# Kernel tuning notes

Hardware: AMD Instinct MI355X
Metric: run time of the kernel (lower is better)

Reference implementation:

```python
import jax, jax.numpy as jnp
import numpy as np

N_NODES = 50000
N_EDGES = 800000
D = 256


def setup_inputs() -> dict:
    key = jax.random.key(0)
    k1, k2, k3 = jax.random.split(key, 3)
    node_features = jax.random.normal(k1, (N_NODES, D), dtype=jnp.float32)
    edge_index = jax.random.randint(k2, (2, N_EDGES), 0, N_NODES, dtype=jnp.int64)
    # GCNConv linear weight (glorot-ish scale) and bias
    W = jax.random.normal(k3, (D, D), dtype=jnp.float32) * (1.0 / np.sqrt(D))
    b = jnp.zeros((D,), dtype=jnp.float32)
    alpha = jnp.full((1,), 0.5, dtype=jnp.float32)
    return {"node_features": node_features, "edge_index": edge_index, "W": W, "b": b, "alpha": alpha}


def _gcn_conv(x, edge_index, W, b):
    # PyG GCNConv: add self-loops, symmetric deg^{-1/2} normalization,
    # x' = W x, out[i] = sum_{j in N(i)} norm_ij * x'_j + b
    N = x.shape[0]
    loop = jnp.arange(N, dtype=edge_index.dtype)
    src = jnp.concatenate([edge_index[0], loop])  # [E+N]
    dst = jnp.concatenate([edge_index[1], loop])
    deg = jax.ops.segment_sum(jnp.ones(src.shape, dtype=x.dtype), dst, num_segments=N)
    dinv = jnp.where(deg > 0, jax.lax.rsqrt(jnp.maximum(deg, 1.0)), 0.0)
    norm = dinv[src] * dinv[dst]  # [E+N]
    h = x @ W.T  # [N, D]
    msg = h[src] * norm[:, None]  # gather + scale
    out = jax.ops.segment_sum(msg, dst, num_segments=N)  # scatter-add to targets
    return out + b


def reference(node_features, edge_index, W, b, alpha):
    updated = _gcn_conv(node_features, edge_index, W, b)
    a = alpha[0]
    # eval mode: dropout = identity; alpha-weighted residual blend
    return a * node_features + (1.0 - a) * updated
```

## Files before the change

### kernel.cpp

```cpp
#include <hip/hip_runtime.h>

#define N_NODES 50000
#define N_EDGES 800000
#define D 256
#define SLOT 64
#define GEMM_BLOCKS 391
#define FILL_BLOCKS 1563

typedef unsigned short bf16_t;
typedef __attribute__((ext_vector_type(8))) short short8;
typedef __attribute__((ext_vector_type(8))) unsigned short ushort8_t;
typedef __attribute__((ext_vector_type(4))) float f32x4;

__device__ inline float b2f(bf16_t u) {
    union { float f; unsigned v; } t; t.v = ((unsigned)u) << 16; return t.f;
}
__device__ inline bf16_t f2b(float f) {
    union { float f; unsigned v; } t; t.f = f;
    unsigned u = t.v;
    return (bf16_t)((u + 0x7FFFu + ((u >> 16) & 1u)) >> 16);
}
__device__ inline unsigned cvt_pk_bf16(float lo, float hi) {
    unsigned r;
    asm("v_cvt_pk_bf16_f32 %0, %1, %2" : "=v"(r) : "v"(lo), "v"(hi));
    return r;
}
__device__ inline short8 cvt8(float4 a, float4 b) {
    union { short8 s; unsigned u[4]; } t;
    t.u[0] = cvt_pk_bf16(a.x, a.y);
    t.u[1] = cvt_pk_bf16(a.z, a.w);
    t.u[2] = cvt_pk_bf16(b.x, b.y);
    t.u[3] = cvt_pk_bf16(b.z, b.w);
    return t.s;
}

__global__ void initcur_kernel(int* __restrict__ cursor) {
    int i = blockIdx.x * 256 + threadIdx.x;
    if (i < N_NODES) cursor[i] = i << 6;
}

__global__ __launch_bounds__(512) void k1_kernel(const float* __restrict__ x,
                                                 const float* __restrict__ W,
                                                 bf16_t* __restrict__ h,
                                                 const int* __restrict__ ei,
                                                 int* __restrict__ cursor,
                                                 int* __restrict__ csr_src) {
    __shared__ __align__(16) bf16_t As[128 * 32];
    __shared__ __align__(16) bf16_t Bs[256 * 32];

    const int tid = threadIdx.x;

    if (blockIdx.x >= GEMM_BLOCKS) {
        int e = (blockIdx.x - GEMM_BLOCKS) * 512 + tid;
        if (e < N_EDGES) {
            int s = ei[e];
            int d = ei[N_EDGES + e];
            if ((unsigned)d < (unsigned)N_NODES) {
                int pos = atomicAdd(&cursor[d], 1);
                csr_src[pos] = s;
            }
        }
        return;
    }

    const int wid  = tid >> 6;
    const int lane = tid & 63;
    const int wr = wid >> 2;
    const int wc = wid & 3;
    const int row0 = blockIdx.x * 128;
    const int lr = lane & 15;
    const int lk = (lane >> 4) * 8;

    const int srow = tid >> 2;
    const int sq   = tid & 3;
    int sr = row0 + srow;
    if (sr >= N_NODES) sr = N_NODES - 1;
    const float* agp = &x[(size_t)sr * D + sq * 8];
    bf16_t* alp = &As[srow * 32 + sq * 8];

    float4 areg[16];
#pragma unroll
    for (int s = 0; s < 8; s++) {
        const float4* p = reinterpret_cast<const float4*>(&agp[s * 32]);
        areg[2 * s]     = p[0];
        areg[2 * s + 1] = p[1];
    }

    f32x4 acc[4][4] = {};

#pragma unroll
    for (int s = 0; s < 8; s++) {
        *reinterpret_cast<short8*>(alp) = cvt8(areg[2 * s], areg[2 * s + 1]);
#pragma unroll
        for (int j = 0; j < 2; j++) {
            int brow = (j * 512 + tid) >> 2;
            const float4* q = reinterpret_cast<const float4*>(&W[(size_t)brow * D + s * 32 + sq * 8]);
            float4 w0 = q[0], w1 = q[1];
            *reinterpret_cast<short8*>(&Bs[brow * 32 + sq * 8]) = cvt8(w0, w1);
        }
        __syncthreads();

        short8 a[4], b[4];
#pragma unroll
        for (int m = 0; m < 4; m++)
            a[m] = *reinterpret_cast<const short8*>(&As[(wr * 64 + m * 16 + lr) * 32 + lk]);
#pragma unroll
        for (int n = 0; n < 4; n++)
            b[n] = *reinterpret_cast<const short8*>(&Bs[(wc * 64 + n * 16 + lr) * 32 + lk]);
#pragma unroll
        for (int m = 0; m < 4; m++)
#pragma unroll
            for (int n = 0; n < 4; n++)
                acc[m][n] = __builtin_amdgcn_mfma_f32_16x16x32_bf16(a[m], b[n], acc[m][n], 0, 0, 0);
        __syncthreads();
    }

#pragma unroll
    for (int m = 0; m < 4; m++) {
        int rbase = row0 + wr * 64 + m * 16 + (lane >> 4) * 4;
#pragma unroll
        for (int j = 0; j < 4; j++) {
            int rr = rbase + j;
            if (rr < N_NODES) {
#pragma unroll
                for (int n = 0; n < 4; n++)
                    h[(size_t)rr * D + wc * 64 + n * 16 + lr] = f2b(acc[m][n][j]);
            }
        }
    }
}

__global__ void dinv_kernel(const int* __restrict__ cursor, float* __restrict__ dinv) {
    int i = blockIdx.x * 256 + threadIdx.x;
    if (i < N_NODES) {
        int cnt = cursor[i] - (i << 6);
        dinv[i] = rsqrtf((float)(cnt + 1));
    }
}

__global__ __launch_bounds__(256) void gather_kernel(const int* __restrict__ cursor,
                                                     const int* __restrict__ csr_src,
                                                     const float* __restrict__ dinv,
                                                     const bf16_t* __restrict__ h,
                                                     const float* __restrict__ x,
                                                     const float* __restrict__ b,
                                                     const float* __restrict__ alpha,
                                                     float* __restrict__ out) {
    const int half = (threadIdx.x >> 5) & 1;
    const int wv   = threadIdx.x >> 6;
    const int ln   = threadIdx.x & 31;
    const int n = blockIdx.x * 8 + wv * 2 + half;
    if (n >= N_NODES) return;
    const int col = ln * 8;

    const int beg = n << 6;
    const int end = cursor[n];
    const float dn = dinv[n];
    const bf16_t* hl = h + col;

    float a0 = 0.f, a1 = 0.f, a2 = 0.f, a3 = 0.f,
          a4 = 0.f, a5 = 0.f, a6 = 0.f, a7 = 0.f;
    int k = beg;
    for (; k + 3 < end; k += 4) {
        int s0 = csr_src[k], s1 = csr_src[k + 1], s2 = csr_src[k + 2], s3 = csr_src[k + 3];
        float n0 = dinv[s0] * dn, n1 = dinv[s1] * dn, n2 = dinv[s2] * dn, n3 = dinv[s3] * dn;
        ushort8_t r0 = *reinterpret_cast<const ushort8_t*>(&hl[(size_t)s0 * D]);
        ushort8_t r1 = *reinterpret_cast<const ushort8_t*>(&hl[(size_t)s1 * D]);
        ushort8_t r2 = *reinterpret_cast<const ushort8_t*>(&hl[(size_t)s2 * D]);
        ushort8_t r3 = *reinterpret_cast<const ushort8_t*>(&hl[(size_t)s3 * D]);
        a0 += b2f(r0[0]) * n0 + b2f(r1[0]) * n1 + b2f(r2[0]) * n2 + b2f(r3[0]) * n3;
        a1 += b2f(r0[1]) * n0 + b2f(r1[1]) * n1 + b2f(r2[1]) * n2 + b2f(r3[1]) * n3;
        a2 += b2f(r0[2]) * n0 + b2f(r1[2]) * n1 + b2f(r2[2]) * n2 + b2f(r3[2]) * n3;
        a3 += b2f(r0[3]) * n0 + b2f(r1[3]) * n1 + b2f(r2[3]) * n2 + b2f(r3[3]) * n3;
        a4 += b2f(r0[4]) * n0 + b2f(r1[4]) * n1 + b2f(r2[4]) * n2 + b2f(r3[4]) * n3;
        a5 += b2f(r0[5]) * n0 + b2f(r1[5]) * n1 + b2f(r2[5]) * n2 + b2f(r3[5]) * n3;
        a6 += b2f(r0[6]) * n0 + b2f(r1[6]) * n1 + b2f(r2[6]) * n2 + b2f(r3[6]) * n3;
        a7 += b2f(r0[7]) * n0 + b2f(r1[7]) * n1 + b2f(r2[7]) * n2 + b2f(r3[7]) * n3;
    }
    for (; k < end; k++) {
        int s0 = csr_src[k];
        float n0 = dinv[s0] * dn;
        ushort8_t r0 = *reinterpret_cast<const ushort8_t*>(&hl[(size_t)s0 * D]);
        a0 += b2f(r0[0]) * n0; a1 += b2f(r0[1]) * n0;
        a2 += b2f(r0[2]) * n0; a3 += b2f(r0[3]) * n0;
        a4 += b2f(r0[4]) * n0; a5 += b2f(r0[5]) * n0;
        a6 += b2f(r0[6]) * n0; a7 += b2f(r0[7]) * n0;
    }

    const float dv2 = dn * dn;
    const float a   = alpha[0];
    ushort8_t hv = *reinterpret_cast<const ushort8_t*>(&hl[(size_t)n * D]);
    const float4* xp = reinterpret_cast<const float4*>(&x[(size_t)n * D + col]);
    const float4* bp = reinterpret_cast<const float4*>(&b[col]);
    float4 xv0 = xp[0], xv1 = xp[1];
    float4 bv0 = bp[0], bv1 = bp[1];
    float4 r0, r1;
    r0.x = a * xv0.x + (1.0f - a) * (a0 + dv2 * b2f(hv[0]) + bv0.x);
    r0.y = a * xv0.y + (1.0f - a) * (a1 + dv2 * b2f(hv[1]) + bv0.y);
    r0.z = a * xv0.z + (1.0f - a) * (a2 + dv2 * b2f(hv[2]) + bv0.z);
    r0.w = a * xv0.w + (1.0f - a) * (a3 + dv2 * b2f(hv[3]) + bv0.w);
    r1.x = a * xv1.x + (1.0f - a) * (a4 + dv2 * b2f(hv[4]) + bv1.x);
    r1.y = a * xv1.y + (1.0f - a) * (a5 + dv2 * b2f(hv[5]) + bv1.y);
    r1.z = a * xv1.z + (1.0f - a) * (a6 + dv2 * b2f(hv[6]) + bv1.z);
    r1.w = a * xv1.w + (1.0f - a) * (a7 + dv2 * b2f(hv[7]) + bv1.w);
    float4* op = reinterpret_cast<float4*>(&out[(size_t)n * D + col]);
    op[0] = r0;
    op[1] = r1;
}

extern "C" void kernel_launch(void* const* d_in, const int* in_sizes, int n_in,
                              void* d_out, int out_size, void* d_ws, size_t ws_size,
                              hipStream_t stream) {
    const float* x     = (const float*)d_in[0];
    const int*   ei    = (const int*)d_in[1];
    const float* W     = (const float*)d_in[2];
    const float* b     = (const float*)d_in[3];
    const float* alpha = (const float*)d_in[4];
    float* out = (float*)d_out;

    char* ws = (char*)d_ws;
    const size_t HB = (size_t)N_NODES * D * 2;
    bf16_t* h      = (bf16_t*)ws;
    int*   cursor  = (int*)  (ws + HB);
    float* dinv    = (float*)(ws + HB + 200000);
    int*   csr_src = (int*)  (ws + HB + 400000);

    initcur_kernel<<<(N_NODES + 255) / 256, 256, 0, stream>>>(cursor);
    k1_kernel<<<GEMM_BLOCKS + FILL_BLOCKS, 512, 0, stream>>>(x, W, h, ei, cursor, csr_src);
    dinv_kernel<<<(N_NODES + 255) / 256, 256, 0, stream>>>(cursor, dinv);
    gather_kernel<<<(N_NODES + 7) / 8, 256, 0, stream>>>(cursor, csr_src, dinv, h, x, b, alpha, out);
}
```

Baseline: 157.2 us.

## Shard per-node edge cursors into sub-buckets and pre-convert W to bf16

Edge bucketing now uses 8 per-node sub-counters (chosen by edge index) with 16 slots each, reducing atomic contention on hot cursors. A new compact kernel packs the sub-buckets contiguously and computes degree and dinv. W is converted to bf16 once in an init kernel instead of per GEMM block, and fill threads process 8 edges each. The price is an extra pass over the CSR, and a sub-bucket overflowing 16 entries would corrupt neighbouring buckets.

Result: faster. 143.5 us (-8.7%).

```diff
diff --git a/kernel.cpp b/kernel.cpp
--- a/kernel.cpp
+++ b/kernel.cpp
@@ -3,9 +3,10 @@
 #define N_NODES 50000
 #define N_EDGES 800000
 #define D 256
-#define SLOT 64
 #define GEMM_BLOCKS 391
-#define FILL_BLOCKS 1563
+#define FILL_BLOCKS 196
+#define CURZ_BLOCKS 1563
+#define WCVT_BLOCKS 32
 
 typedef unsigned short bf16_t;
 typedef __attribute__((ext_vector_type(8))) short short8;
@@ -34,30 +35,49 @@
     return t.s;
 }
 
-__global__ void initcur_kernel(int* __restrict__ cursor) {
-    int i = blockIdx.x * 256 + threadIdx.x;
-    if (i < N_NODES) cursor[i] = i << 6;
+__global__ __launch_bounds__(256) void init_kernel(const float* __restrict__ W,
+                                                   int* __restrict__ cursor,
+                                                   bf16_t* __restrict__ Wb) {
+    const int tid = threadIdx.x;
+    int bid = blockIdx.x;
+    if (bid < CURZ_BLOCKS) {
+        int i = bid * 256 + tid;
+        if (i < N_NODES * 8) cursor[i] = 0;
+        return;
+    }
+    bid -= CURZ_BLOCKS;
+    {
+        int i = bid * 256 + tid;
+        const float4* p = reinterpret_cast<const float4*>(W) + (size_t)i * 2;
+        float4 v0 = p[0], v1 = p[1];
+        *reinterpret_cast<short8*>(&Wb[(size_t)i * 8]) = cvt8(v0, v1);
+    }
 }
 
 __global__ __launch_bounds__(512) void k1_kernel(const float* __restrict__ x,
-                                                 const float* __restrict__ W,
+                                                 const bf16_t* __restrict__ Wb,
                                                  bf16_t* __restrict__ h,
                                                  const int* __restrict__ ei,
                                                  int* __restrict__ cursor,
-                                                 int* __restrict__ csr_src) {
+                                                 int* __restrict__ csr) {
     __shared__ __align__(16) bf16_t As[128 * 32];
     __shared__ __align__(16) bf16_t Bs[256 * 32];
 
     const int tid = threadIdx.x;
 
     if (blockIdx.x >= GEMM_BLOCKS) {
-        int e = (blockIdx.x - GEMM_BLOCKS) * 512 + tid;
-        if (e < N_EDGES) {
-            int s = ei[e];
-            int d = ei[N_EDGES + e];
-            if ((unsigned)d < (unsigned)N_NODES) {
-                int pos = atomicAdd(&cursor[d], 1);
-                csr_src[pos] = s;
+        int e0 = (blockIdx.x - GEMM_BLOCKS) * 4096 + tid;
+#pragma unroll
+        for (int j = 0; j < 8; j++) {
+            int e = e0 + j * 512;
+            if (e < N_EDGES) {
+                int s = ei[e];
+                int d = ei[N_EDGES + e];
+                if ((unsigned)d < (unsigned)N_NODES) {
+                    int sh = e & 7;
+                    int r = atomicAdd(&cursor[d * 8 + sh], 1);
+                    csr[(d << 7) + (sh << 4) + r] = s;
+                }
             }
         }
         return;
@@ -94,9 +114,8 @@
 #pragma unroll
         for (int j = 0; j < 2; j++) {
             int brow = (j * 512 + tid) >> 2;
-            const float4* q = reinterpret_cast<const float4*>(&W[(size_t)brow * D + s * 32 + sq * 8]);
-            float4 w0 = q[0], w1 = q[1];
-            *reinterpret_cast<short8*>(&Bs[brow * 32 + sq * 8]) = cvt8(w0, w1);
+            short8 wv = *reinterpret_cast<const short8*>(&Wb[(size_t)brow * D + s * 32 + sq * 8]);
+            *reinterpret_cast<short8*>(&Bs[brow * 32 + sq * 8]) = wv;
         }
         __syncthreads();
 
@@ -130,16 +149,46 @@
     }
 }
 
-__global__ void dinv_kernel(const int* __restrict__ cursor, float* __restrict__ dinv) {
-    int i = blockIdx.x * 256 + threadIdx.x;
-    if (i < N_NODES) {
-        int cnt = cursor[i] - (i << 6);
-        dinv[i] = rsqrtf((float)(cnt + 1));
-    }
-}
-
-__global__ __launch_bounds__(256) void gather_kernel(const int* __restrict__ cursor,
-                                                     const int* __restrict__ csr_src,
+__global__ __launch_bounds__(256) void compact_kernel(const int* __restrict__ cursor,
+                                                      int* __restrict__ csr,
+                                                      int* __restrict__ degarr,
+                                                      float* __restrict__ dinv) {
+    const int grp = threadIdx.x >> 5;
+    const int ln  = threadIdx.x & 31;
+    const int n = blockIdx.x * 8 + grp;
+    if (n >= N_NODES) return;
+
+    const int4* cp = reinterpret_cast<const int4*>(&cursor[n * 8]);
+    int4 ca = cp[0], cb = cp[1];
+    int c[8] = {ca.x, ca.y, ca.z, ca.w, cb.x, cb.y, cb.z, cb.w};
+    int p[8];
+    int acc = 0;
+#pragma unroll
+    for (int j = 0; j < 8; j++) { p[j] = acc; acc += c[j]; }
+    const int base = n << 7;
+
+    int vals[4], dsts[4];
+    bool ok[4];
+#pragma unroll
+    for (int t = 0; t < 4; t++) {
+        int slot = ln + t * 32;
+        int j = slot >> 4, r = slot & 15;
+        ok[t] = (r < c[j]);
+        vals[t] = ok[t] ? csr[base + slot] : 0;
+        dsts[t] = base + p[j] + r;
+    }
+#pragma unroll
+    for (int t = 0; t < 4; t++)
+        if (ok[t]) csr[dsts[t]] = vals[t];
+
+    if (ln == 0) {
+        degarr[n] = acc;
+        dinv[n] = rsqrtf((float)(acc + 1));
+    }
+}
+
+__global__ __launch_bounds__(256) void gather_kernel(const int* __restrict__ degarr,
+                                                     const int* __restrict__ csr,
                                                      const float* __restrict__ dinv,
                                                      const bf16_t* __restrict__ h,
                                                      const float* __restrict__ x,
@@ -153,8 +202,8 @@
     if (n >= N_NODES) return;
     const int col = ln * 8;
 
-    const int beg = n << 6;
-    const int end = cursor[n];
+    const int beg = n << 7;
+    const int end = beg + degarr[n];
     const float dn = dinv[n];
     const bf16_t* hl = h + col;
 
@@ -162,7 +211,7 @@
           a4 = 0.f, a5 = 0.f, a6 = 0.f, a7 = 0.f;
     int k = beg;
     for (; k + 3 < end; k += 4) {
-        int s0 = csr_src[k], s1 = csr_src[k + 1], s2 = csr_src[k + 2], s3 = csr_src[k + 3];
+        int s0 = csr[k], s1 = csr[k + 1], s2 = csr[k + 2], s3 = csr[k + 3];
         float n0 = dinv[s0] * dn, n1 = dinv[s1] * dn, n2 = dinv[s2] * dn, n3 = dinv[s3] * dn;
         ushort8_t r0 = *reinterpret_cast<const ushort8_t*>(&hl[(size_t)s0 * D]);
         ushort8_t r1 = *reinterpret_cast<const ushort8_t*>(&hl[(size_t)s1 * D]);
@@ -178,7 +227,7 @@
         a7 += b2f(r0[7]) * n0 + b2f(r1[7]) * n1 + b2f(r2[7]) * n2 + b2f(r3[7]) * n3;
     }
     for (; k < end; k++) {
-        int s0 = csr_src[k];
+        int s0 = csr[k];
         float n0 = dinv[s0] * dn;
         ushort8_t r0 = *reinterpret_cast<const ushort8_t*>(&hl[(size_t)s0 * D]);
         a0 += b2f(r0[0]) * n0; a1 += b2f(r0[1]) * n0;
@@ -188,24 +237,24 @@
     }
 
     const float dv2 = dn * dn;
-    const float a   = alpha[0];
+    const float av  = alpha[0];
     ushort8_t hv = *reinterpret_cast<const ushort8_t*>(&hl[(size_t)n * D]);
     const float4* xp = reinterpret_cast<const float4*>(&x[(size_t)n * D + col]);
     const float4* bp = reinterpret_cast<const float4*>(&b[col]);
     float4 xv0 = xp[0], xv1 = xp[1];
     float4 bv0 = bp[0], bv1 = bp[1];
-    float4 r0, r1;
-    r0.x = a * xv0.x + (1.0f - a) * (a0 + dv2 * b2f(hv[0]) + bv0.x);
-    r0.y = a * xv0.y + (1.0f - a) * (a1 + dv2 * b2f(hv[1]) + bv0.y);
-    r0.z = a * xv0.z + (1.0f - a) * (a2 + dv2 * b2f(hv[2]) + bv0.z);
-    r0.w = a * xv0.w + (1.0f - a) * (a3 + dv2 * b2f(hv[3]) + bv0.w);
-    r1.x = a * xv1.x + (1.0f - a) * (a4 + dv2 * b2f(hv[4]) + bv1.x);
-    r1.y = a * xv1.y + (1.0f - a) * (a5 + dv2 * b2f(hv[5]) + bv1.y);
-    r1.z = a * xv1.z + (1.0f - a) * (a6 + dv2 * b2f(hv[6]) + bv1.z);
-    r1.w = a * xv1.w + (1.0f - a) * (a7 + dv2 * b2f(hv[7]) + bv1.w);
+    float4 o0, o1;
+    o0.x = av * xv0.x + (1.0f - av) * (a0 + dv2 * b2f(hv[0]) + bv0.x);
+    o0.y = av * xv0.y + (1.0f - av) * (a1 + dv2 * b2f(hv[1]) + bv0.y);
+    o0.z = av * xv0.z + (1.0f - av) * (a2 + dv2 * b2f(hv[2]) + bv0.z);
+    o0.w = av * xv0.w + (1.0f - av) * (a3 + dv2 * b2f(hv[3]) + bv0.w);
+    o1.x = av * xv1.x + (1.0f - av) * (a4 + dv2 * b2f(hv[4]) + bv1.x);
+    o1.y = av * xv1.y + (1.0f - av) * (a5 + dv2 * b2f(hv[5]) + bv1.y);
+    o1.z = av * xv1.z + (1.0f - av) * (a6 + dv2 * b2f(hv[6]) + bv1.z);
+    o1.w = av * xv1.w + (1.0f - av) * (a7 + dv2 * b2f(hv[7]) + bv1.w);
     float4* op = reinterpret_cast<float4*>(&out[(size_t)n * D + col]);
-    op[0] = r0;
-    op[1] = r1;
+    op[0] = o0;
+    op[1] = o1;
 }
 
 extern "C" void kernel_launch(void* const* d_in, const int* in_sizes, int n_in,
@@ -219,14 +268,15 @@
     float* out = (float*)d_out;
 
     char* ws = (char*)d_ws;
-    const size_t HB = (size_t)N_NODES * D * 2;
     bf16_t* h      = (bf16_t*)ws;
-    int*   cursor  = (int*)  (ws + HB);
-    float* dinv    = (float*)(ws + HB + 200000);
-    int*   csr_src = (int*)  (ws + HB + 400000);
-
-    initcur_kernel<<<(N_NODES + 255) / 256, 256, 0, stream>>>(cursor);
-    k1_kernel<<<GEMM_BLOCKS + FILL_BLOCKS, 512, 0, stream>>>(x, W, h, ei, cursor, csr_src);
-    dinv_kernel<<<(N_NODES + 255) / 256, 256, 0, stream>>>(cursor, dinv);
-    gather_kernel<<<(N_NODES + 7) / 8, 256, 0, stream>>>(cursor, csr_src, dinv, h, x, b, alpha, out);
-}
+    bf16_t* Wb     = (bf16_t*)(ws + 25600000);
+    int*   cursor  = (int*)  (ws + 25731072);
+    float* dinv    = (float*)(ws + 27331072);
+    int*   degarr  = (int*)  (ws + 27531072);
+    int*   csr     = (int*)  (ws + 27731072);
+
+    init_kernel<<<CURZ_BLOCKS + WCVT_BLOCKS, 256, 0, stream>>>(W, cursor, Wb);
+    k1_kernel<<<GEMM_BLOCKS + FILL_BLOCKS, 512, 0, stream>>>(x, Wb, h, ei, cursor, csr);
+    compact_kernel<<<(N_NODES + 7) / 8, 256, 0, stream>>>(cursor, csr, degarr, dinv);
+    gather_kernel<<<(N_NODES + 7) / 8, 256, 0, stream>>>(degarr, csr, dinv, h, x, b, alpha, out);
+}
```
